# Performance work log

Measured on AMD Instinct MI355X. Metric: run time of the kernel, lower is better.

Reference implementation:

```python
import jax, jax.numpy as jnp
import numpy as np

K = 2          # kernel_size
NQ = K * K     # n_qubits = 4
DEPTH = 2      # quantum_depth


def _zmat(n):
    # zmat[k, i] = +1 if bit of wire i (wire 0 = MSB, PennyLane convention) is 0, else -1
    dim = 2 ** n
    bits = np.array([[(k >> (n - 1 - i)) & 1 for i in range(n)] for k in range(dim)])
    return jnp.asarray(1 - 2 * bits, dtype=jnp.float32)  # [2^n, n]


def _cnot_perm(n, entanglement):
    # basis-state permutation implementing one entangling layer of CNOTs
    if entanglement == 'full':
        pairs = [(i, i + 1) for i in range(n - 1)] + [(n - 1, 0)]
    else:  # 'pair'
        pairs = [(i, i + 1) for i in range(0, n, 2)]
    dim = 2 ** n
    perm = np.zeros(dim, dtype=np.int64)
    for k in range(dim):
        bits = [(k >> (n - 1 - i)) & 1 for i in range(n)]
        for c, t in pairs:
            bits[t] ^= bits[c]
        m = 0
        for i in range(n):
            m = (m << 1) | bits[i]
        perm[m] = k  # state'[m] = state[k]  =>  state' = state[:, perm]
    return jnp.asarray(perm)


_ZMAT = _zmat(NQ)                  # [16, 4]
_PERM = _cnot_perm(NQ, 'full')     # [16]


def quantum_expvals(angles, qparams):
    """Batched 4-qubit statevector sim.
    angles: [N, NQ] RX rotation angles; qparams: [DEPTH, NQ] RZ angles.
    Returns [N] expval of PauliZ(wire 0)."""
    N = angles.shape[0]
    c = jnp.cos(angles * 0.5)
    s = jnp.sin(angles * 0.5)
    # RX on |0>: [cos(a/2), -i sin(a/2)]; build product state (wire 0 = MSB)
    state = jnp.ones((N, 1), dtype=jnp.complex64)
    for i in range(NQ):
        q = jnp.stack([c[:, i] + 0j, -1j * s[:, i]], axis=-1)  # [N, 2]
        state = (state[:, :, None] * q[:, None, :]).reshape(N, -1)
    # depth layers: fused RZ diagonal over all wires, then CNOT permutation
    for d in range(qparams.shape[0]):
        diag = jnp.exp(-0.5j * (_ZMAT @ qparams[d]).astype(jnp.complex64))  # [16]
        state = state * diag[None, :]
        state = state[:, _PERM]
    probs = state.real ** 2 + state.imag ** 2
    return jnp.sum(probs * _ZMAT[:, 0][None, :], axis=1)  # <Z_0>


def reference(x, conv_w, conv_b, qparams):
    # classical: Conv2d(1,1,2,bias) -> ReLU
    cls = jax.lax.conv_general_dilated(
        x, conv_w, window_strides=(1, 1), padding='VALID',
        dimension_numbers=('NCHW', 'OIHW', 'NCHW'))
    cls = jax.nn.relu(cls + conv_b.reshape(1, -1, 1, 1))
    B, C, H, W = cls.shape
    Hp, Wp = H // K, W // K
    # non-overlapping KxK patches, row-major within patch (matches torch unfold+view)
    patches = cls[:, 0, :Hp * K, :Wp * K].reshape(B, Hp, K, Wp, K)
    patches = patches.transpose(0, 1, 3, 2, 4).reshape(B * Hp * Wp, K * K)
    qvals = quantum_expvals(patches, qparams).reshape(B, 1, Hp, Wp)
    # nearest-neighbor upsample by K
    qmap = jnp.repeat(jnp.repeat(qvals, K, axis=2), K, axis=3)
    return jnp.concatenate([cls, qmap], axis=1)  # [B, 2, H, W]


def setup_inputs() -> dict:
    key = jax.random.key(0)
    k1, k2, k3, k4 = jax.random.split(key, 4)
    return {
        'x': jax.random.normal(k1, (64, 1, 257, 257), dtype=jnp.float32),
        'conv_w': jax.random.normal(k2, (1, 1, K, K), dtype=jnp.float32),
        'conv_b': jax.random.normal(k3, (1,), dtype=jnp.float32),
        'qparams': jax.random.normal(k4, (DEPTH, NQ), dtype=jnp.float32),
    }
```

## Files before the change

### kernel.cpp

```cpp
#include <hip/hip_runtime.h>


#define BATCH 64
#define INH   257
#define INW   257
#define OH    256
#define OW    256
#define RG    32
#define LROWS 9
#define LPITCH 264

typedef float fvec4 __attribute__((ext_vector_type(4)));

__device__ __forceinline__ void store_nt4(float* p, float x, float y, float z, float w)
{
    fvec4 v; v.x = x; v.y = y; v.z = z; v.w = w;
    __builtin_nontemporal_store(v, (fvec4*)p);
}

__global__ __launch_bounds__(256) void conv_enh_lds(
    const float* __restrict__ x,
    const float* __restrict__ cw,
    const float* __restrict__ cb,
    float* __restrict__ out)
{
    __shared__ float lds[LROWS * LPITCH];

    const int tid = threadIdx.x;
    const int blk = blockIdx.x;
    const int rg  = blk & (RG - 1);
    const int b   = blk >> 5;

    const float w00 = cw[0], w01 = cw[1], w10 = cw[2], w11 = cw[3];
    const float bias = cb[0];

    const int r_base = rg * 8;
    const float* __restrict__ src =
        x + (size_t)b * INH * INW + (size_t)r_base * INW;

    #pragma unroll
    for (int r = 0; r < LROWS; ++r)
        lds[r * LPITCH + tid] = src[r * INW + tid];
    if (tid < LROWS)
        lds[tid * LPITCH + 256] = src[tid * INW + 256];
    __syncthreads();

    const int j  = tid & 63;
    const int il = tid >> 6;
    const int c0 = 4 * j;

    const float* __restrict__ l0 = &lds[(2 * il) * LPITCH + c0];
    const float* __restrict__ l1 = l0 + LPITCH;
    const float* __restrict__ l2 = l1 + LPITCH;

    const fvec4 A = *(const fvec4*)l0;  const float a4 = l0[4];
    const fvec4 M = *(const fvec4*)l1;  const float m4 = l1[4];
    const fvec4 Z = *(const fvec4*)l2;  const float z4 = l2[4];

    const float t0 = fmaxf(fmaf(w11, M.y, fmaf(w10, M.x, fmaf(w01, A.y, fmaf(w00, A.x, bias)))), 0.f);
    const float t1 = fmaxf(fmaf(w11, M.z, fmaf(w10, M.y, fmaf(w01, A.z, fmaf(w00, A.y, bias)))), 0.f);
    const float t2 = fmaxf(fmaf(w11, M.w, fmaf(w10, M.z, fmaf(w01, A.w, fmaf(w00, A.z, bias)))), 0.f);
    const float t3 = fmaxf(fmaf(w11, m4,  fmaf(w10, M.w, fmaf(w01, a4,  fmaf(w00, A.w, bias)))), 0.f);
    const float u0 = fmaxf(fmaf(w11, Z.y, fmaf(w10, Z.x, fmaf(w01, M.y, fmaf(w00, M.x, bias)))), 0.f);
    const float u1 = fmaxf(fmaf(w11, Z.z, fmaf(w10, Z.y, fmaf(w01, M.z, fmaf(w00, M.y, bias)))), 0.f);
    const float u2 = fmaxf(fmaf(w11, Z.w, fmaf(w10, Z.z, fmaf(w01, M.w, fmaf(w00, M.z, bias)))), 0.f);
    const float u3 = fmaxf(fmaf(w11, z4,  fmaf(w10, Z.w, fmaf(w01, m4,  fmaf(w00, M.w, bias)))), 0.f);

    const float q0 = __cosf(t0) * __cosf(t1) * __cosf(u1);
    const float q1 = __cosf(t2) * __cosf(t3) * __cosf(u3);

    const int r0 = r_base + 2 * il;
    float* __restrict__ o0 = out + (size_t)b * 2 * OH * OW + (size_t)r0 * OW + c0;
    float* __restrict__ o1 = o0 + OH * OW;

    store_nt4(o0,      t0, t1, t2, t3);
    store_nt4(o0 + OW, u0, u1, u2, u3);
    store_nt4(o1,      q0, q0, q1, q1);
    store_nt4(o1 + OW, q0, q0, q1, q1);
}

extern "C" void kernel_launch(void* const* d_in, const int* in_sizes, int n_in,
                              void* d_out, int out_size, void* d_ws, size_t ws_size,
                              hipStream_t stream)
{
    const float* x  = (const float*)d_in[0];
    const float* cw = (const float*)d_in[1];
    const float* cb = (const float*)d_in[2];
    float* out = (float*)d_out;

    const int grid  = BATCH * RG;
    const int block = 256;
    conv_enh_lds<<<grid, block, 0, stream>>>(x, cw, cb, out);
}
```

Before: 79.78 us.

## Process four row groups per block with double-buffered LDS prefetch

Each block now handles four consecutive 8-row groups instead of one. The next group's input rows are loaded into registers while the current group is computed from LDS, then written into the alternate LDS buffer. This is meant to overlap global-load latency with compute and stores, and to amortise block setup. In exchange the grid shrinks fourfold, which reduces resident waves available to hide memory latency.

```diff
diff --git a/kernel.cpp b/kernel.cpp
--- a/kernel.cpp
+++ b/kernel.cpp
@@ -6,9 +6,10 @@
 #define INW   257
 #define OH    256
 #define OW    256
-#define RG    32
 #define LROWS 9
 #define LPITCH 264
+#define GPB   4
+#define MACROS 8
 
 typedef float fvec4 __attribute__((ext_vector_type(4)));
 
@@ -18,65 +19,89 @@
     __builtin_nontemporal_store(v, (fvec4*)p);
 }
 
-__global__ __launch_bounds__(256) void conv_enh_lds(
+__global__ __launch_bounds__(256) void conv_enh_pipe(
     const float* __restrict__ x,
     const float* __restrict__ cw,
     const float* __restrict__ cb,
     float* __restrict__ out)
 {
-    __shared__ float lds[LROWS * LPITCH];
+    __shared__ float lds[2][LROWS * LPITCH];
 
     const int tid = threadIdx.x;
     const int blk = blockIdx.x;
-    const int rg  = blk & (RG - 1);
-    const int b   = blk >> 5;
+    const int m   = blk & (MACROS - 1);
+    const int b   = blk >> 3;
 
     const float w00 = cw[0], w01 = cw[1], w10 = cw[2], w11 = cw[3];
     const float bias = cb[0];
 
-    const int r_base = rg * 8;
-    const float* __restrict__ src =
-        x + (size_t)b * INH * INW + (size_t)r_base * INW;
-
-    #pragma unroll
-    for (int r = 0; r < LROWS; ++r)
-        lds[r * LPITCH + tid] = src[r * INW + tid];
-    if (tid < LROWS)
-        lds[tid * LPITCH + 256] = src[tid * INW + 256];
-    __syncthreads();
-
+    const float* __restrict__ img = x + (size_t)b * INH * INW;
     const int j  = tid & 63;
     const int il = tid >> 6;
     const int c0 = 4 * j;
 
-    const float* __restrict__ l0 = &lds[(2 * il) * LPITCH + c0];
-    const float* __restrict__ l1 = l0 + LPITCH;
-    const float* __restrict__ l2 = l1 + LPITCH;
+    {
+        const float* __restrict__ s = img + (size_t)(m * 32) * INW;
+        #pragma unroll
+        for (int r = 0; r < LROWS; ++r)
+            lds[0][r * LPITCH + tid] = s[r * INW + tid];
+        if (tid < LROWS)
+            lds[0][tid * LPITCH + 256] = s[tid * INW + 256];
+    }
+    __syncthreads();
 
-    const fvec4 A = *(const fvec4*)l0;  const float a4 = l0[4];
-    const fvec4 M = *(const fvec4*)l1;  const float m4 = l1[4];
-    const fvec4 Z = *(const fvec4*)l2;  const float z4 = l2[4];
+    float reg[LROWS];
+    float rhalo = 0.f;
 
-    const float t0 = fmaxf(fmaf(w11, M.y, fmaf(w10, M.x, fmaf(w01, A.y, fmaf(w00, A.x, bias)))), 0.f);
-    const float t1 = fmaxf(fmaf(w11, M.z, fmaf(w10, M.y, fmaf(w01, A.z, fmaf(w00, A.y, bias)))), 0.f);
-    const float t2 = fmaxf(fmaf(w11, M.w, fmaf(w10, M.z, fmaf(w01, A.w, fmaf(w00, A.z, bias)))), 0.f);
-    const float t3 = fmaxf(fmaf(w11, m4,  fmaf(w10, M.w, fmaf(w01, a4,  fmaf(w00, A.w, bias)))), 0.f);
-    const float u0 = fmaxf(fmaf(w11, Z.y, fmaf(w10, Z.x, fmaf(w01, M.y, fmaf(w00, M.x, bias)))), 0.f);
-    const float u1 = fmaxf(fmaf(w11, Z.z, fmaf(w10, Z.y, fmaf(w01, M.z, fmaf(w00, M.y, bias)))), 0.f);
-    const float u2 = fmaxf(fmaf(w11, Z.w, fmaf(w10, Z.z, fmaf(w01, M.w, fmaf(w00, M.z, bias)))), 0.f);
-    const float u3 = fmaxf(fmaf(w11, z4,  fmaf(w10, Z.w, fmaf(w01, m4,  fmaf(w00, M.w, bias)))), 0.f);
+    #pragma unroll
+    for (int g = 0; g < GPB; ++g) {
+        if (g + 1 < GPB) {
+            const float* __restrict__ s = img + (size_t)(m * 32 + (g + 1) * 8) * INW;
+            #pragma unroll
+            for (int r = 0; r < LROWS; ++r)
+                reg[r] = s[r * INW + tid];
+            rhalo = (tid < LROWS) ? s[tid * INW + 256] : 0.f;
+        }
 
-    const float q0 = __cosf(t0) * __cosf(t1) * __cosf(u1);
-    const float q1 = __cosf(t2) * __cosf(t3) * __cosf(u3);
+        const float* __restrict__ l0 = &lds[g & 1][(2 * il) * LPITCH + c0];
+        const float* __restrict__ l1 = l0 + LPITCH;
+        const float* __restrict__ l2 = l1 + LPITCH;
 
-    const int r0 = r_base + 2 * il;
-    float* __restrict__ o0 = out + (size_t)b * 2 * OH * OW + (size_t)r0 * OW + c0;
-    float* __restrict__ o1 = o0 + OH * OW;
+        const fvec4 A = *(const fvec4*)l0;  const float a4 = l0[4];
+        const fvec4 M = *(const fvec4*)l1;  const float m4 = l1[4];
+        const fvec4 Z = *(const fvec4*)l2;  const float z4 = l2[4];
 
-    store_nt4(o0,      t0, t1, t2, t3);
-    store_nt4(o0 + OW, u0, u1, u2, u3);
-    store_nt4(o1,      q0, q0, q1, q1);
-    store_nt4(o1 + OW, q0, q0, q1, q1);
+        const float t0 = fmaxf(fmaf(w11, M.y, fmaf(w10, M.x, fmaf(w01, A.y, fmaf(w00, A.x, bias)))), 0.f);
+        const float t1 = fmaxf(fmaf(w11, M.z, fmaf(w10, M.y, fmaf(w01, A.z, fmaf(w00, A.y, bias)))), 0.f);
+        const float t2 = fmaxf(fmaf(w11, M.w, fmaf(w10, M.z, fmaf(w01, A.w, fmaf(w00, A.z, bias)))), 0.f);
+        const float t3 = fmaxf(fmaf(w11, m4,  fmaf(w10, M.w, fmaf(w01, a4,  fmaf(w00, A.w, bias)))), 0.f);
+        const float u0 = fmaxf(fmaf(w11, Z.y, fmaf(w10, Z.x, fmaf(w01, M.y, fmaf(w00, M.x, bias)))), 0.f);
+        const float u1 = fmaxf(fmaf(w11, Z.z, fmaf(w10, Z.y, fmaf(w01, M.z, fmaf(w00, M.y, bias)))), 0.f);
+        const float u2 = fmaxf(fmaf(w11, Z.w, fmaf(w10, Z.z, fmaf(w01, M.w, fmaf(w00, M.z, bias)))), 0.f);
+        const float u3 = fmaxf(fmaf(w11, z4,  fmaf(w10, Z.w, fmaf(w01, m4,  fmaf(w00, M.w, bias)))), 0.f);
+
+        const float q0 = __cosf(t0) * __cosf(t1) * __cosf(u1);
+        const float q1 = __cosf(t2) * __cosf(t3) * __cosf(u3);
+
+        const int r0 = m * 32 + g * 8 + 2 * il;
+        float* __restrict__ o0 = out + (size_t)b * 2 * OH * OW + (size_t)r0 * OW + c0;
+        float* __restrict__ o1 = o0 + OH * OW;
+
+        store_nt4(o0,      t0, t1, t2, t3);
+        store_nt4(o0 + OW, u0, u1, u2, u3);
+        store_nt4(o1,      q0, q0, q1, q1);
+        store_nt4(o1 + OW, q0, q0, q1, q1);
+
+        if (g + 1 < GPB) {
+            float* __restrict__ d = lds[(g + 1) & 1];
+            #pragma unroll
+            for (int r = 0; r < LROWS; ++r)
+                d[r * LPITCH + tid] = reg[r];
+            if (tid < LROWS)
+                d[tid * LPITCH + 256] = rhalo;
+            __syncthreads();
+        }
+    }
 }
 
 extern "C" void kernel_launch(void* const* d_in, const int* in_sizes, int n_in,
@@ -88,7 +113,7 @@
     const float* cb = (const float*)d_in[2];
     float* out = (float*)d_out;
 
-    const int grid  = BATCH * RG;
+    const int grid  = BATCH * MACROS;
     const int block = 256;
-    conv_enh_lds<<<grid, block, 0, stream>>>(x, cw, cb, out);
+    conv_enh_pipe<<<grid, block, 0, stream>>>(x, cw, cb, out);
 }
```

Result: no change. 78.73 us (-1.3%).
